# Kernel tuning notes

Measured on AMD Instinct MI355X. Metric: run time of the kernel, lower is better.

Reference implementation:

```python
import jax, jax.numpy as jnp
import numpy as np

G = 14       # patch_size
K = 4        # patch_amount
SCALE = 2    # scale_factor (undefined global in source; canonical RAM value)
C = 1
EPS = 1e-5   # torch BatchNorm1d default eps


def extract_patch(x, loc, size):
    # x: (B, C, H, W), loc in [-1, 1]. Always pad (zero-pad is value-equivalent
    # to the source's conditional padding) then gather with dynamic_slice.
    B, C_, H, W = x.shape
    pad = size // 2 + 1
    xp = jnp.pad(x, ((0, 0), (0, 0), (pad, pad), (pad, pad)))
    coords = (0.5 * ((loc + 1.0) * H)).astype(jnp.int32)  # denormalize -> (B,2) [x, y]
    x0 = coords[:, 0] - size // 2 + pad
    y0 = coords[:, 1] - size // 2 + pad

    def slice_one(img, yy, xx):
        return jax.lax.dynamic_slice(img, (0, yy, xx), (C_, size, size))

    return jax.vmap(slice_one)(xp, y0, x0)  # (B, C, size, size)


def foveate(x, loc):
    patches = []
    size = G
    for _ in range(K):
        p = extract_patch(x, loc, size)
        k = size // G
        if k > 1:  # F.avg_pool2d(p, k)
            B, C_, s, _ = p.shape
            p = p.reshape(B, C_, G, k, G, k).mean(axis=(3, 5))
        patches.append(p)
        size = int(SCALE * size)
    phi = jnp.concatenate(patches, axis=1)  # (B, K*C, G, G)
    return phi.reshape(phi.shape[0], -1)    # (B, 784)


def batchnorm(h, gamma, beta):
    # training-mode BatchNorm1d: batch stats, biased variance
    m = h.mean(axis=0)
    v = h.var(axis=0)
    return (h - m) * jax.lax.rsqrt(v + EPS) * gamma + beta


def mlp(h, W1, b1, g1, be1, W2, b2, g2, be2):
    h = jax.nn.relu(batchnorm(h @ W1 + b1, g1, be1))
    return batchnorm(h @ W2 + b2, g2, be2)


def setup_inputs() -> dict:
    key = jax.random.key(0)
    ks = jax.random.split(key, 8)
    B, H = 4096, 128
    x = jax.random.uniform(ks[0], (B, C, H, H), dtype=jnp.float32)
    loc = jax.random.uniform(ks[1], (B, 2), minval=-1.0, maxval=1.0, dtype=jnp.float32)

    def lin(k, fi, fo):
        return jax.random.normal(k, (fi, fo), dtype=jnp.float32) * 0.05

    d = {"x": x, "loc": loc}
    d["what_W1"] = lin(ks[2], 784, 128); d["what_b1"] = jnp.zeros((128,), jnp.float32)
    d["what_g1"] = jnp.ones((128,), jnp.float32); d["what_be1"] = jnp.zeros((128,), jnp.float32)
    d["what_W2"] = lin(ks[3], 128, 256); d["what_b2"] = jnp.zeros((256,), jnp.float32)
    d["what_g2"] = jnp.ones((256,), jnp.float32); d["what_be2"] = jnp.zeros((256,), jnp.float32)
    d["where_W1"] = lin(ks[4], 2, 128); d["where_b1"] = jnp.zeros((128,), jnp.float32)
    d["where_g1"] = jnp.ones((128,), jnp.float32); d["where_be1"] = jnp.zeros((128,), jnp.float32)
    d["where_W2"] = lin(ks[5], 128, 256); d["where_b2"] = jnp.zeros((256,), jnp.float32)
    d["where_g2"] = jnp.ones((256,), jnp.float32); d["where_be2"] = jnp.zeros((256,), jnp.float32)
    return d


def reference(x, loc, what_W1, what_b1, what_g1, what_be1, what_W2, what_b2, what_g2, what_be2, where_W1, where_b1, where_g1, where_be1, where_W2, where_b2, where_g2, where_be2):
    phi = foveate(x, loc)  # (B, 784)
    res_phi = mlp(phi, what_W1, what_b1, what_g1, what_be1, what_W2, what_b2, what_g2, what_be2)
    res_k = mlp(loc, where_W1, where_b1, where_g1, where_be1, where_W2, where_b2, where_g2, where_be2)
    return jax.nn.relu(res_phi + res_k)  # (B, 256)
```

## Files before the change

kernel.cpp:

```cpp
#include <hip/hip_runtime.h>
#include <hip/hip_bf16.h>

typedef __hip_bfloat16 bf16;

static constexpr int kB = 4096;
static constexpr float kEPS = 1e-5f;

__device__ __forceinline__ float cvt(float v) { return v; }
__device__ __forceinline__ float cvt(bf16 v)  { return __bfloat162float(v); }

__device__ __forceinline__ int detect_dtype(const void* __restrict__ x) {
    const bf16* p = (const bf16*)x;
    int isf32 = 0;
    for (int i = 0; i < 64; ++i) {
        float v = __bfloat162float(p[i]);
        if (!(fabsf(v) <= 2.0f)) isf32 = 1;
    }
    return isf32;
}

template <typename T>
__device__ void foveate_impl(const T* __restrict__ x, const T* __restrict__ loc,
                             float* __restrict__ phi, float* __restrict__ L1,
                             float* __restrict__ L2) {
    int b = blockIdx.x;
    float lx = cvt(loc[2 * b + 0]);
    float ly = cvt(loc[2 * b + 1]);
    int cx = (int)(0.5f * ((lx + 1.0f) * 128.0f));
    int cy = (int)(0.5f * ((ly + 1.0f) * 128.0f));
    const T* img = x + (size_t)b * 16384;
    float* ph = phi + (size_t)b * 784;

    int by0 = cy - 56, bx0 = cx - 56;
    for (int i = threadIdx.x; i < 56 * 56; i += 256) {
        int oy = i / 56, ox = i - oy * 56;
        int gy = by0 + 2 * oy, gx = bx0 + 2 * ox;
        float v00 = ((unsigned)gy       < 128u && (unsigned)gx       < 128u) ? cvt(img[gy * 128 + gx])           : 0.f;
        float v01 = ((unsigned)gy       < 128u && (unsigned)(gx + 1) < 128u) ? cvt(img[gy * 128 + gx + 1])       : 0.f;
        float v10 = ((unsigned)(gy + 1) < 128u && (unsigned)gx       < 128u) ? cvt(img[(gy + 1) * 128 + gx])     : 0.f;
        float v11 = ((unsigned)(gy + 1) < 128u && (unsigned)(gx + 1) < 128u) ? cvt(img[(gy + 1) * 128 + gx + 1]) : 0.f;
        L1[oy * 57 + ox] = ((v00 + v01) + v10) + v11;
    }
    __syncthreads();

    for (int i = threadIdx.x; i < 196; i += 256) {
        int r = i / 14, c = i % 14;
        int gy = cy - 7 + r, gx = cx - 7 + c;
        float v = ((unsigned)gy < 128u && (unsigned)gx < 128u) ? cvt(img[gy * 128 + gx]) : 0.f;
        ph[i] = v;
        ph[196 + i] = L1[(21 + r) * 57 + 21 + c] * 0.25f;
    }
    for (int i = threadIdx.x; i < 784; i += 256) {
        int oy = i / 28, ox = i % 28;
        const float* p = L1 + (2 * oy) * 57 + 2 * ox;
        L2[oy * 29 + ox] = p[0] + p[1] + p[57] + p[58];
    }
    __syncthreads();

    for (int i = threadIdx.x; i < 196; i += 256) {
        int r = i / 14, c = i % 14;
        ph[392 + i] = L2[(7 + r) * 29 + 7 + c] * 0.0625f;
        const float* p = L2 + (2 * r) * 29 + 2 * c;
        ph[588 + i] = (p[0] + p[1] + p[29] + p[30]) * 0.015625f;
    }
}

__global__ __launch_bounds__(256) void foveate_kernel(const void* __restrict__ x,
                                                      const void* __restrict__ loc,
                                                      float* __restrict__ phi,
                                                      int* __restrict__ flag) {
    __shared__ float L1[56 * 57];
    __shared__ float L2[28 * 29];
    int isf32 = detect_dtype(x);
    if (blockIdx.x == 0 && threadIdx.x == 0) *flag = isf32;
    if (isf32) foveate_impl<float>((const float*)x, (const float*)loc, phi, L1, L2);
    else       foveate_impl<bf16>((const bf16*)x, (const bf16*)loc, phi, L1, L2);
}

template <typename T>
__device__ void gemm1_impl(const float* __restrict__ A, const T* __restrict__ W,
                           const T* __restrict__ bias, float* __restrict__ C,
                           float* __restrict__ part_s, float* __restrict__ part_q,
                           float* As, float* Bs) {
    int tid = threadIdx.x;
    int tx = tid & 15, ty = tid >> 4;
    int row0 = blockIdx.y * 64, n0 = blockIdx.x * 32;

    float acc[4][2] = {};
    int am = tid >> 2;
    int ak = (tid & 3) << 2;
    int bn = tid & 31;
    int bk = tid >> 5;

    const float* Aptr = A + (size_t)(row0 + am) * 784 + ak;
    float4 av = *(const float4*)Aptr;
    float b0 = cvt(W[(size_t)bk * 128 + n0 + bn]);
    float b1 = cvt(W[(size_t)(bk + 8) * 128 + n0 + bn]);

    for (int t = 0; t < 49; ++t) {
        As[(ak + 0) * 68 + am] = av.x; As[(ak + 1) * 68 + am] = av.y;
        As[(ak + 2) * 68 + am] = av.z; As[(ak + 3) * 68 + am] = av.w;
        Bs[bk * 32 + bn] = b0; Bs[(bk + 8) * 32 + bn] = b1;
        __syncthreads();
        if (t < 48) {
            int k0 = (t + 1) << 4;
            av = *(const float4*)(Aptr + k0);
            b0 = cvt(W[(size_t)(k0 + bk) * 128 + n0 + bn]);
            b1 = cvt(W[(size_t)(k0 + bk + 8) * 128 + n0 + bn]);
        }
#pragma unroll
        for (int k = 0; k < 16; ++k) {
            float4 a  = *(const float4*)&As[k * 68 + ty * 4];
            float2 bb = *(const float2*)&Bs[k * 32 + tx * 2];
            acc[0][0] = fmaf(a.x, bb.x, acc[0][0]); acc[0][1] = fmaf(a.x, bb.y, acc[0][1]);
            acc[1][0] = fmaf(a.y, bb.x, acc[1][0]); acc[1][1] = fmaf(a.y, bb.y, acc[1][1]);
            acc[2][0] = fmaf(a.z, bb.x, acc[2][0]); acc[2][1] = fmaf(a.z, bb.y, acc[2][1]);
            acc[3][0] = fmaf(a.w, bb.x, acc[3][0]); acc[3][1] = fmaf(a.w, bb.y, acc[3][1]);
        }
        __syncthreads();
    }

    float bv0 = cvt(bias[n0 + tx * 2]);
    float bv1 = cvt(bias[n0 + tx * 2 + 1]);
    float cs0 = 0.f, cs1 = 0.f, cq0 = 0.f, cq1 = 0.f;
#pragma unroll
    for (int i = 0; i < 4; ++i) {
        float v0 = acc[i][0] + bv0, v1 = acc[i][1] + bv1;
        float2 o; o.x = v0; o.y = v1;
        *(float2*)(C + (size_t)(row0 + ty * 4 + i) * 128 + n0 + tx * 2) = o;
        cs0 += v0; cq0 += v0 * v0; cs1 += v1; cq1 += v1 * v1;
    }
    __syncthreads();
    As[ty * 32 + tx * 2]     = cs0; As[ty * 32 + tx * 2 + 1] = cs1;
    Bs[ty * 32 + tx * 2]     = cq0; Bs[ty * 32 + tx * 2 + 1] = cq1;
    __syncthreads();
    if (tid < 32) {
        float s = 0.f, q = 0.f;
#pragma unroll
        for (int p = 0; p < 16; ++p) { s += As[p * 32 + tid]; q += Bs[p * 32 + tid]; }
        part_s[(size_t)blockIdx.y * 128 + n0 + tid] = s;
        part_q[(size_t)blockIdx.y * 128 + n0 + tid] = q;
    }
}

__global__ __launch_bounds__(256) void gemm1_fused(const float* __restrict__ A,
                                                   const void* __restrict__ W,
                                                   const void* __restrict__ bias,
                                                   float* __restrict__ C,
                                                   float* __restrict__ part_s,
                                                   float* __restrict__ part_q,
                                                   const int* __restrict__ flag) {
    __shared__ __align__(16) float As[16 * 68];
    __shared__ __align__(16) float Bs[16 * 32];
    if (*flag) gemm1_impl<float>(A, (const float*)W, (const float*)bias, C, part_s, part_q, As, Bs);
    else       gemm1_impl<bf16>(A, (const bf16*)W, (const bf16*)bias, C, part_s, part_q, As, Bs);
}

template <typename T>
__device__ void where1_impl(const T* __restrict__ loc, const T* __restrict__ W,
                            const T* __restrict__ bias, float* __restrict__ q1,
                            float* __restrict__ part_s, float* __restrict__ part_q,
                            float* redS, float* redQ) {
    int c    = threadIdx.x & 127;
    int rsub = threadIdx.x >> 7;
    int rbase = blockIdx.x * 64;
    float w0 = cvt(W[c]), w1 = cvt(W[128 + c]), bv = cvt(bias[c]);
    float s = 0.f, q = 0.f;
#pragma unroll
    for (int p = 0; p < 32; ++p) {
        int r = rbase + rsub + 2 * p;
        float v = fmaf(cvt(loc[2 * r]), w0, fmaf(cvt(loc[2 * r + 1]), w1, bv));
        q1[(size_t)r * 128 + c] = v;
        s += v; q += v * v;
    }
    redS[threadIdx.x] = s; redQ[threadIdx.x] = q;
    __syncthreads();
    if (threadIdx.x < 128) {
        part_s[(size_t)blockIdx.x * 128 + c] = redS[c] + redS[c + 128];
        part_q[(size_t)blockIdx.x * 128 + c] = redQ[c] + redQ[c + 128];
    }
}

__global__ __launch_bounds__(256) void where1_fused(const void* __restrict__ loc,
                                                    const void* __restrict__ W,
                                                    const void* __restrict__ bias,
                                                    float* __restrict__ q1,
                                                    float* __restrict__ part_s,
                                                    float* __restrict__ part_q,
                                                    const int* __restrict__ flag) {
    __shared__ float redS[256], redQ[256];
    if (*flag) where1_impl<float>((const float*)loc, (const float*)W, (const float*)bias, q1, part_s, part_q, redS, redQ);
    else       where1_impl<bf16>((const bf16*)loc, (const bf16*)W, (const bf16*)bias, q1, part_s, part_q, redS, redQ);
}

template <typename T>
__device__ void fin_impl(const float* __restrict__ pS, const float* __restrict__ pQ,
                         const T* __restrict__ g, const T* __restrict__ be,
                         float* __restrict__ st) {
    int c = threadIdx.x;
    double s = 0.0, q = 0.0;
    for (int p = 0; p < 64; ++p) {
        s += (double)pS[p * 128 + c];
        q += (double)pQ[p * 128 + c];
    }
    double mean = s / 4096.0;
    double var  = q / 4096.0 - mean * mean;
    float rstd  = (float)(1.0 / sqrt(var + (double)kEPS));
    float scale = rstd * cvt(g[c]);
    st[c]       = scale;
    st[128 + c] = cvt(be[c]) - (float)mean * scale;
}

__global__ __launch_bounds__(128) void finalize_both(
        const float* __restrict__ pS1, const float* __restrict__ pQ1,
        const void* __restrict__ g1, const void* __restrict__ be1, float* __restrict__ st1,
        const float* __restrict__ pSw1, const float* __restrict__ pQw1,
        const void* __restrict__ gw1, const void* __restrict__ bew1, float* __restrict__ sw1,
        const int* __restrict__ flag) {
    const float* pS = blockIdx.x ? pSw1 : pS1;
    const float* pQ = blockIdx.x ? pQw1 : pQ1;
    const void*  g  = blockIdx.x ? gw1  : g1;
    const void*  be = blockIdx.x ? bew1 : be1;
    float* st       = blockIdx.x ? sw1  : st1;
    if (*flag) fin_impl<float>(pS, pQ, (const float*)g, (const float*)be, st);
    else       fin_impl<bf16>(pS, pQ, (const bf16*)g, (const bf16*)be, st);
}

template <typename T>
__device__ void gemm2_impl(const float* __restrict__ A, const T* __restrict__ W,
                           const T* __restrict__ bias, const float* __restrict__ st,
                           float* __restrict__ C, float* __restrict__ part_s,
                           float* __restrict__ part_q, float* As, float* Bs) {
    int tid = threadIdx.x;
    int tx = tid & 15, ty = tid >> 4;
    int row0 = blockIdx.y * 64, n0 = blockIdx.x * 64;

    float acc[4][4] = {};
    int am = tid >> 2, ak = (tid & 3) << 2;
    int bn = tid & 63, bk0 = tid >> 6;

    const float* Aptr = A + (size_t)(row0 + am) * 128 + ak;
    float4 av = *(const float4*)Aptr;
    float4 sc = *(const float4*)(st + ak);
    float4 sh = *(const float4*)(st + 128 + ak);
    float bv[4];
#pragma unroll
    for (int p = 0; p < 4; ++p) bv[p] = cvt(W[(size_t)(bk0 + 4 * p) * 256 + n0 + bn]);

    for (int t = 0; t < 8; ++t) {
        As[(ak + 0) * 68 + am] = fmaxf(fmaf(av.x, sc.x, sh.x), 0.f);
        As[(ak + 1) * 68 + am] = fmaxf(fmaf(av.y, sc.y, sh.y), 0.f);
        As[(ak + 2) * 68 + am] = fmaxf(fmaf(av.z, sc.z, sh.z), 0.f);
        As[(ak + 3) * 68 + am] = fmaxf(fmaf(av.w, sc.w, sh.w), 0.f);
#pragma unroll
        for (int p = 0; p < 4; ++p) Bs[(bk0 + 4 * p) * 64 + bn] = bv[p];
        __syncthreads();
        if (t < 7) {
            int k0 = (t + 1) << 4;
            av = *(const float4*)(Aptr + k0);
            sc = *(const float4*)(st + k0 + ak);
            sh = *(const float4*)(st + 128 + k0 + ak);
#pragma unroll
            for (int p = 0; p < 4; ++p) bv[p] = cvt(W[(size_t)(k0 + bk0 + 4 * p) * 256 + n0 + bn]);
        }
#pragma unroll
        for (int k = 0; k < 16; ++k) {
            float4 a = *(const float4*)&As[k * 68 + ty * 4];
            float4 b = *(const float4*)&Bs[k * 64 + tx * 4];
            acc[0][0] = fmaf(a.x, b.x, acc[0][0]); acc[0][1] = fmaf(a.x, b.y, acc[0][1]);
            acc[0][2] = fmaf(a.x, b.z, acc[0][2]); acc[0][3] = fmaf(a.x, b.w, acc[0][3]);
            acc[1][0] = fmaf(a.y, b.x, acc[1][0]); acc[1][1] = fmaf(a.y, b.y, acc[1][1]);
            acc[1][2] = fmaf(a.y, b.z, acc[1][2]); acc[1][3] = fmaf(a.y, b.w, acc[1][3]);
            acc[2][0] = fmaf(a.z, b.x, acc[2][0]); acc[2][1] = fmaf(a.z, b.y, acc[2][1]);
            acc[2][2] = fmaf(a.z, b.z, acc[2][2]); acc[2][3] = fmaf(a.z, b.w, acc[2][3]);
            acc[3][0] = fmaf(a.w, b.x, acc[3][0]); acc[3][1] = fmaf(a.w, b.y, acc[3][1]);
            acc[3][2] = fmaf(a.w, b.z, acc[3][2]); acc[3][3] = fmaf(a.w, b.w, acc[3][3]);
        }
        __syncthreads();
    }

    float bb[4];
#pragma unroll
    for (int j = 0; j < 4; ++j) bb[j] = cvt(bias[n0 + tx * 4 + j]);
    float cs[4] = {}, cq[4] = {};
#pragma unroll
    for (int i = 0; i < 4; ++i) {
        float v0 = acc[i][0] + bb[0], v1 = acc[i][1] + bb[1];
        float v2 = acc[i][2] + bb[2], v3 = acc[i][3] + bb[3];
        float4 o; o.x = v0; o.y = v1; o.z = v2; o.w = v3;
        cs[0] += v0; cs[1] += v1; cs[2] += v2; cs[3] += v3;
        cq[0] += v0 * v0; cq[1] += v1 * v1; cq[2] += v2 * v2; cq[3] += v3 * v3;
        *(float4*)(C + (size_t)(row0 + ty * 4 + i) * 256 + n0 + tx * 4) = o;
    }
    __syncthreads();
#pragma unroll
    for (int j = 0; j < 4; ++j) {
        As[ty * 64 + tx * 4 + j] = cs[j];
        Bs[ty * 64 + tx * 4 + j] = cq[j];
    }
    __syncthreads();
    if (tid < 64) {
        float s = 0.f, q = 0.f;
#pragma unroll
        for (int p = 0; p < 16; ++p) { s += As[p * 64 + tid]; q += Bs[p * 64 + tid]; }
        part_s[(size_t)blockIdx.y * 256 + n0 + tid] = s;
        part_q[(size_t)blockIdx.y * 256 + n0 + tid] = q;
    }
}

__global__ __launch_bounds__(256) void gemm23_fused(
        const float* __restrict__ h1, const float* __restrict__ q1,
        const void* __restrict__ wW2, const void* __restrict__ wb2,
        const void* __restrict__ hW2, const void* __restrict__ hb2,
        const float* __restrict__ st1, const float* __restrict__ sw1,
        float* __restrict__ h2, float* __restrict__ q2,
        float* __restrict__ pS2, float* __restrict__ pQ2,
        float* __restrict__ pSw2, float* __restrict__ pQw2,
        const int* __restrict__ flag) {
    __shared__ __align__(16) float As[16 * 68];
    __shared__ __align__(16) float Bs[16 * 64];
    const float* A;  const void* W; const void* bias; const float* st;
    float* C; float* ps; float* pq;
    if (blockIdx.z == 0) { A = h1; W = wW2; bias = wb2; st = st1; C = h2; ps = pS2;  pq = pQ2;  }
    else                 { A = q1; W = hW2; bias = hb2; st = sw1; C = q2; ps = pSw2; pq = pQw2; }
    if (*flag) gemm2_impl<float>(A, (const float*)W, (const float*)bias, st, C, ps, pq, As, Bs);
    else       gemm2_impl<bf16>(A, (const bf16*)W, (const bf16*)bias, st, C, ps, pq, As, Bs);
}

template <typename T>
__device__ void final_impl(const float* __restrict__ h2, const float* __restrict__ q2,
                           const float* __restrict__ pS2, const float* __restrict__ pQ2,
                           const float* __restrict__ pSw2, const float* __restrict__ pQw2,
                           const T* __restrict__ g2, const T* __restrict__ be2,
                           const T* __restrict__ gw2, const T* __restrict__ bew2,
                           T* __restrict__ out) {
    int c = threadIdx.x;
    double s = 0.0, q = 0.0, sw = 0.0, qw = 0.0;
    for (int p = 0; p < 64; ++p) {
        s  += (double)pS2[p * 256 + c];  q  += (double)pQ2[p * 256 + c];
        sw += (double)pSw2[p * 256 + c]; qw += (double)pQw2[p * 256 + c];
    }
    double mH = s / 4096.0,  vH = q / 4096.0 - mH * mH;
    double mQ = sw / 4096.0, vQ = qw / 4096.0 - mQ * mQ;
    float rH = (float)(1.0 / sqrt(vH + (double)kEPS));
    float rQ = (float)(1.0 / sqrt(vQ + (double)kEPS));
    float aH = rH * cvt(g2[c]);  float bH = cvt(be2[c])  - (float)mH * aH;
    float aQ = rQ * cvt(gw2[c]); float bQ = cvt(bew2[c]) - (float)mQ * aQ;

    for (int idx = blockIdx.x * 256 + c; idx < kB * 256; idx += 256 * 256) {
        float v = fmaxf(fmaf(h2[idx], aH, bH) + fmaf(q2[idx], aQ, bQ), 0.f);
        out[idx] = (T)v;
    }
}

__global__ __launch_bounds__(256) void final_kernel(
        const float* __restrict__ h2, const float* __restrict__ q2,
        const float* __restrict__ pS2, const float* __restrict__ pQ2,
        const float* __restrict__ pSw2, const float* __restrict__ pQw2,
        const void* __restrict__ g2, const void* __restrict__ be2,
        const void* __restrict__ gw2, const void* __restrict__ bew2,
        void* __restrict__ out, const int* __restrict__ flag) {
    if (*flag) final_impl<float>(h2, q2, pS2, pQ2, pSw2, pQw2, (const float*)g2, (const float*)be2,
                                 (const float*)gw2, (const float*)bew2, (float*)out);
    else       final_impl<bf16>(h2, q2, pS2, pQ2, pSw2, pQw2, (const bf16*)g2, (const bf16*)be2,
                                (const bf16*)gw2, (const bf16*)bew2, (bf16*)out);
}

extern "C" void kernel_launch(void* const* d_in, const int* in_sizes, int n_in,
                              void* d_out, int out_size, void* d_ws, size_t ws_size,
                              hipStream_t stream) {
    (void)in_sizes; (void)n_in; (void)out_size; (void)ws_size;
    const void* x    = d_in[0];
    const void* loc  = d_in[1];
    const void* wW1  = d_in[2];
    const void* wb1  = d_in[3];
    const void* wg1  = d_in[4];
    const void* wbe1 = d_in[5];
    const void* wW2  = d_in[6];
    const void* wb2  = d_in[7];
    const void* wg2  = d_in[8];
    const void* wbe2 = d_in[9];
    const void* hW1  = d_in[10];
    const void* hb1  = d_in[11];
    const void* hg1  = d_in[12];
    const void* hbe1 = d_in[13];
    const void* hW2  = d_in[14];
    const void* hb2  = d_in[15];
    const void* hg2  = d_in[16];
    const void* hbe2 = d_in[17];

    int*   flag = (int*)d_ws;
    float* ws   = (float*)d_ws + 16;
    float* phi  = ws;
    float* h1   = phi + (size_t)kB * 784;
    float* q1   = h1  + (size_t)kB * 128;
    float* h2   = q1  + (size_t)kB * 128;
    float* q2   = h2  + (size_t)kB * 256;
    float* st1  = q2  + (size_t)kB * 256;
    float* sw1  = st1 + 256;
    float* pS1  = sw1 + 256;
    float* pQ1  = pS1 + 8192;
    float* pSw1 = pQ1 + 8192;
    float* pQw1 = pSw1 + 8192;
    float* pS2  = phi;
    float* pQ2  = pS2 + 16384;
    float* pSw2 = pQ2 + 16384;
    float* pQw2 = pSw2 + 16384;

    foveate_kernel<<<kB, 256, 0, stream>>>(x, loc, phi, flag);

    gemm1_fused<<<dim3(4, 64), 256, 0, stream>>>(phi, wW1, wb1, h1, pS1, pQ1, flag);
    where1_fused<<<64, 256, 0, stream>>>(loc, hW1, hb1, q1, pSw1, pQw1, flag);

    finalize_both<<<2, 128, 0, stream>>>(pS1, pQ1, wg1, wbe1, st1,
                                         pSw1, pQw1, hg1, hbe1, sw1, flag);

    gemm23_fused<<<dim3(4, 64, 2), 256, 0, stream>>>(h1, q1, wW2, wb2, hW2, hb2,
                                                     st1, sw1, h2, q2,
                                                     pS2, pQ2, pSw2, pQw2, flag);

    final_kernel<<<256, 256, 0, stream>>>(h2, q2, pS2, pQ2, pSw2, pQw2,
                                          wg2, wbe2, hg2, hbe2, d_out, flag);
}
```

Baseline: 437.2 us.

## Fuse foveation with first what-GEMM and where-layer into one kernel

```diff
diff --git a/kernel.cpp b/kernel.cpp
--- a/kernel.cpp
+++ b/kernel.cpp
@@ -20,150 +20,130 @@
 }
 
 template <typename T>
-__device__ void foveate_impl(const T* __restrict__ x, const T* __restrict__ loc,
-                             float* __restrict__ phi, float* __restrict__ L1,
-                             float* __restrict__ L2) {
-    int b = blockIdx.x;
-    float lx = cvt(loc[2 * b + 0]);
-    float ly = cvt(loc[2 * b + 1]);
-    int cx = (int)(0.5f * ((lx + 1.0f) * 128.0f));
-    int cy = (int)(0.5f * ((ly + 1.0f) * 128.0f));
-    const T* img = x + (size_t)b * 16384;
-    float* ph = phi + (size_t)b * 784;
-
-    int by0 = cy - 56, bx0 = cx - 56;
-    for (int i = threadIdx.x; i < 56 * 56; i += 256) {
-        int oy = i / 56, ox = i - oy * 56;
-        int gy = by0 + 2 * oy, gx = bx0 + 2 * ox;
-        float v00 = ((unsigned)gy       < 128u && (unsigned)gx       < 128u) ? cvt(img[gy * 128 + gx])           : 0.f;
-        float v01 = ((unsigned)gy       < 128u && (unsigned)(gx + 1) < 128u) ? cvt(img[gy * 128 + gx + 1])       : 0.f;
-        float v10 = ((unsigned)(gy + 1) < 128u && (unsigned)gx       < 128u) ? cvt(img[(gy + 1) * 128 + gx])     : 0.f;
-        float v11 = ((unsigned)(gy + 1) < 128u && (unsigned)(gx + 1) < 128u) ? cvt(img[(gy + 1) * 128 + gx + 1]) : 0.f;
-        L1[oy * 57 + ox] = ((v00 + v01) + v10) + v11;
-    }
-    __syncthreads();
-
-    for (int i = threadIdx.x; i < 196; i += 256) {
-        int r = i / 14, c = i % 14;
-        int gy = cy - 7 + r, gx = cx - 7 + c;
-        float v = ((unsigned)gy < 128u && (unsigned)gx < 128u) ? cvt(img[gy * 128 + gx]) : 0.f;
-        ph[i] = v;
-        ph[196 + i] = L1[(21 + r) * 57 + 21 + c] * 0.25f;
-    }
-    for (int i = threadIdx.x; i < 784; i += 256) {
-        int oy = i / 28, ox = i % 28;
-        const float* p = L1 + (2 * oy) * 57 + 2 * ox;
-        L2[oy * 29 + ox] = p[0] + p[1] + p[57] + p[58];
-    }
-    __syncthreads();
-
-    for (int i = threadIdx.x; i < 196; i += 256) {
-        int r = i / 14, c = i % 14;
-        ph[392 + i] = L2[(7 + r) * 29 + 7 + c] * 0.0625f;
-        const float* p = L2 + (2 * r) * 29 + 2 * c;
-        ph[588 + i] = (p[0] + p[1] + p[29] + p[30]) * 0.015625f;
-    }
-}
-
-__global__ __launch_bounds__(256) void foveate_kernel(const void* __restrict__ x,
-                                                      const void* __restrict__ loc,
-                                                      float* __restrict__ phi,
-                                                      int* __restrict__ flag) {
-    __shared__ float L1[56 * 57];
-    __shared__ float L2[28 * 29];
-    int isf32 = detect_dtype(x);
-    if (blockIdx.x == 0 && threadIdx.x == 0) *flag = isf32;
-    if (isf32) foveate_impl<float>((const float*)x, (const float*)loc, phi, L1, L2);
-    else       foveate_impl<bf16>((const bf16*)x, (const bf16*)loc, phi, L1, L2);
-}
-
-template <typename T>
-__device__ void gemm1_impl(const float* __restrict__ A, const T* __restrict__ W,
-                           const T* __restrict__ bias, float* __restrict__ C,
-                           float* __restrict__ part_s, float* __restrict__ part_q,
-                           float* As, float* Bs) {
+__device__ void fovgemm_impl(const T* __restrict__ x, const T* __restrict__ loc,
+                             const T* __restrict__ W1, const T* __restrict__ b1,
+                             float* __restrict__ h1, float* __restrict__ pS,
+                             float* __restrict__ pQ, float* S) {
+    float* phiL = S;
+    float* L1b  = S + 6272;
+    float* Wt   = L1b;
     int tid = threadIdx.x;
-    int tx = tid & 15, ty = tid >> 4;
-    int row0 = blockIdx.y * 64, n0 = blockIdx.x * 32;
-
-    float acc[4][2] = {};
-    int am = tid >> 2;
-    int ak = (tid & 3) << 2;
-    int bn = tid & 31;
-    int bk = tid >> 5;
-
-    const float* Aptr = A + (size_t)(row0 + am) * 784 + ak;
-    float4 av = *(const float4*)Aptr;
-    float b0 = cvt(W[(size_t)bk * 128 + n0 + bn]);
-    float b1 = cvt(W[(size_t)(bk + 8) * 128 + n0 + bn]);
+    int bb  = blockIdx.x;
+    int r0  = bb * 8;
+
+    for (int img = 0; img < 8; ++img) {
+        int b = r0 + img;
+        float lx = cvt(loc[2 * b + 0]);
+        float ly = cvt(loc[2 * b + 1]);
+        int cx = (int)(0.5f * ((lx + 1.0f) * 128.0f));
+        int cy = (int)(0.5f * ((ly + 1.0f) * 128.0f));
+        const T* im = x + (size_t)b * 16384;
+        float* ph = phiL + img * 784;
+
+        int by0 = cy - 56, bx0 = cx - 56;
+        for (int i = tid; i < 56 * 56; i += 256) {
+            int oy = i / 56, ox = i - oy * 56;
+            int gy = by0 + 2 * oy, gx = bx0 + 2 * ox;
+            float v00 = ((unsigned)gy       < 128u && (unsigned)gx       < 128u) ? cvt(im[gy * 128 + gx])           : 0.f;
+            float v01 = ((unsigned)gy       < 128u && (unsigned)(gx + 1) < 128u) ? cvt(im[gy * 128 + gx + 1])       : 0.f;
+            float v10 = ((unsigned)(gy + 1) < 128u && (unsigned)gx       < 128u) ? cvt(im[(gy + 1) * 128 + gx])     : 0.f;
+            float v11 = ((unsigned)(gy + 1) < 128u && (unsigned)(gx + 1) < 128u) ? cvt(im[(gy + 1) * 128 + gx + 1]) : 0.f;
+            L1b[oy * 56 + ox] = ((v00 + v01) + v10) + v11;
+        }
+        __syncthreads();
+
+        for (int i = tid; i < 196; i += 256) {
+            int r = i / 14, c = i % 14;
+            int gy = cy - 7 + r, gx = cx - 7 + c;
+            ph[i] = ((unsigned)gy < 128u && (unsigned)gx < 128u) ? cvt(im[gy * 128 + gx]) : 0.f;
+            ph[196 + i] = L1b[(21 + r) * 56 + 21 + c] * 0.25f;
+
+            auto L2v = [&](int oy, int ox) {
+                const float* q = L1b + (2 * oy) * 56 + 2 * ox;
+                return ((q[0] + q[1]) + q[56]) + q[57];
+            };
+            ph[392 + i] = L2v(7 + r, 7 + c) * 0.0625f;
+            float A0 = L2v(2 * r, 2 * c),     A1 = L2v(2 * r, 2 * c + 1);
+            float A2 = L2v(2 * r + 1, 2 * c), A3 = L2v(2 * r + 1, 2 * c + 1);
+            ph[588 + i] = (((A0 + A1) + A2) + A3) * 0.015625f;
+        }
+        __syncthreads();
+    }
+
+    int tr = tid >> 5;
+    int tc = tid & 31;
+    float acc[4] = {};
+    float wreg[8];
+#pragma unroll
+    for (int j8 = 0; j8 < 8; ++j8) {
+        int j = tid + 256 * j8;
+        wreg[j8] = cvt(W1[(size_t)(j >> 7) * 128 + (j & 127)]);
+    }
 
     for (int t = 0; t < 49; ++t) {
-        As[(ak + 0) * 68 + am] = av.x; As[(ak + 1) * 68 + am] = av.y;
-        As[(ak + 2) * 68 + am] = av.z; As[(ak + 3) * 68 + am] = av.w;
-        Bs[bk * 32 + bn] = b0; Bs[(bk + 8) * 32 + bn] = b1;
+#pragma unroll
+        for (int j8 = 0; j8 < 8; ++j8) Wt[tid + 256 * j8] = wreg[j8];
         __syncthreads();
         if (t < 48) {
             int k0 = (t + 1) << 4;
-            av = *(const float4*)(Aptr + k0);
-            b0 = cvt(W[(size_t)(k0 + bk) * 128 + n0 + bn]);
-            b1 = cvt(W[(size_t)(k0 + bk + 8) * 128 + n0 + bn]);
-        }
-#pragma unroll
-        for (int k = 0; k < 16; ++k) {
-            float4 a  = *(const float4*)&As[k * 68 + ty * 4];
-            float2 bb = *(const float2*)&Bs[k * 32 + tx * 2];
-            acc[0][0] = fmaf(a.x, bb.x, acc[0][0]); acc[0][1] = fmaf(a.x, bb.y, acc[0][1]);
-            acc[1][0] = fmaf(a.y, bb.x, acc[1][0]); acc[1][1] = fmaf(a.y, bb.y, acc[1][1]);
-            acc[2][0] = fmaf(a.z, bb.x, acc[2][0]); acc[2][1] = fmaf(a.z, bb.y, acc[2][1]);
-            acc[3][0] = fmaf(a.w, bb.x, acc[3][0]); acc[3][1] = fmaf(a.w, bb.y, acc[3][1]);
-        }
-        __syncthreads();
-    }
-
-    float bv0 = cvt(bias[n0 + tx * 2]);
-    float bv1 = cvt(bias[n0 + tx * 2 + 1]);
-    float cs0 = 0.f, cs1 = 0.f, cq0 = 0.f, cq1 = 0.f;
-#pragma unroll
-    for (int i = 0; i < 4; ++i) {
-        float v0 = acc[i][0] + bv0, v1 = acc[i][1] + bv1;
-        float2 o; o.x = v0; o.y = v1;
-        *(float2*)(C + (size_t)(row0 + ty * 4 + i) * 128 + n0 + tx * 2) = o;
-        cs0 += v0; cq0 += v0 * v0; cs1 += v1; cq1 += v1 * v1;
-    }
+#pragma unroll
+            for (int j8 = 0; j8 < 8; ++j8) {
+                int j = tid + 256 * j8;
+                wreg[j8] = cvt(W1[(size_t)(k0 + (j >> 7)) * 128 + (j & 127)]);
+            }
+        }
+        const float* ap = phiL + tr * 784 + (t << 4);
+#pragma unroll
+        for (int k4 = 0; k4 < 4; ++k4) {
+            float4 a = *(const float4*)(ap + 4 * k4);
+            const float* wb = Wt + (4 * k4) * 128 + 4 * tc;
+            float4 b0 = *(const float4*)(wb);
+            float4 b1v = *(const float4*)(wb + 128);
+            float4 b2 = *(const float4*)(wb + 256);
+            float4 b3 = *(const float4*)(wb + 384);
+            acc[0] = fmaf(a.x, b0.x, acc[0]); acc[1] = fmaf(a.x, b0.y, acc[1]);
+            acc[2] = fmaf(a.x, b0.z, acc[2]); acc[3] = fmaf(a.x, b0.w, acc[3]);
+            acc[0] = fmaf(a.y, b1v.x, acc[0]); acc[1] = fmaf(a.y, b1v.y, acc[1]);
+            acc[2] = fmaf(a.y, b1v.z, acc[2]); acc[3] = fmaf(a.y, b1v.w, acc[3]);
+            acc[0] = fmaf(a.z, b2.x, acc[0]); acc[1] = fmaf(a.z, b2.y, acc[1]);
+            acc[2] = fmaf(a.z, b2.z, acc[2]); acc[3] = fmaf(a.z, b2.w, acc[3]);
+            acc[0] = fmaf(a.w, b3.x, acc[0]); acc[1] = fmaf(a.w, b3.y, acc[1]);
+            acc[2] = fmaf(a.w, b3.z, acc[2]); acc[3] = fmaf(a.w, b3.w, acc[3]);
+        }
+        __syncthreads();
+    }
+
+    float v0 = acc[0] + cvt(b1[4 * tc + 0]);
+    float v1 = acc[1] + cvt(b1[4 * tc + 1]);
+    float v2 = acc[2] + cvt(b1[4 * tc + 2]);
+    float v3 = acc[3] + cvt(b1[4 * tc + 3]);
+    float4 o; o.x = v0; o.y = v1; o.z = v2; o.w = v3;
+    *(float4*)(h1 + (size_t)(r0 + tr) * 128 + 4 * tc) = o;
+
+    float* redS = phiL;
+    float* redQ = phiL + 1024;
+    float4 cs; cs.x = v0; cs.y = v1; cs.z = v2; cs.w = v3;
+    float4 cq; cq.x = v0 * v0; cq.y = v1 * v1; cq.z = v2 * v2; cq.w = v3 * v3;
+    *(float4*)&redS[tr * 128 + 4 * tc] = cs;
+    *(float4*)&redQ[tr * 128 + 4 * tc] = cq;
     __syncthreads();
-    As[ty * 32 + tx * 2]     = cs0; As[ty * 32 + tx * 2 + 1] = cs1;
-    Bs[ty * 32 + tx * 2]     = cq0; Bs[ty * 32 + tx * 2 + 1] = cq1;
-    __syncthreads();
-    if (tid < 32) {
+    if (tid < 128) {
         float s = 0.f, q = 0.f;
 #pragma unroll
-        for (int p = 0; p < 16; ++p) { s += As[p * 32 + tid]; q += Bs[p * 32 + tid]; }
-        part_s[(size_t)blockIdx.y * 128 + n0 + tid] = s;
-        part_q[(size_t)blockIdx.y * 128 + n0 + tid] = q;
-    }
-}
-
-__global__ __launch_bounds__(256) void gemm1_fused(const float* __restrict__ A,
-                                                   const void* __restrict__ W,
-                                                   const void* __restrict__ bias,
-                                                   float* __restrict__ C,
-                                                   float* __restrict__ part_s,
-                                                   float* __restrict__ part_q,
-                                                   const int* __restrict__ flag) {
-    __shared__ __align__(16) float As[16 * 68];
-    __shared__ __align__(16) float Bs[16 * 32];
-    if (*flag) gemm1_impl<float>(A, (const float*)W, (const float*)bias, C, part_s, part_q, As, Bs);
-    else       gemm1_impl<bf16>(A, (const bf16*)W, (const bf16*)bias, C, part_s, part_q, As, Bs);
+        for (int p = 0; p < 8; ++p) { s += redS[p * 128 + tid]; q += redQ[p * 128 + tid]; }
+        pS[(size_t)bb * 128 + tid] = s;
+        pQ[(size_t)bb * 128 + tid] = q;
+    }
 }
 
 template <typename T>
 __device__ void where1_impl(const T* __restrict__ loc, const T* __restrict__ W,
                             const T* __restrict__ bias, float* __restrict__ q1,
                             float* __restrict__ part_s, float* __restrict__ part_q,
-                            float* redS, float* redQ) {
+                            float* redS, float* redQ, int wb) {
     int c    = threadIdx.x & 127;
     int rsub = threadIdx.x >> 7;
-    int rbase = blockIdx.x * 64;
+    int rbase = wb * 64;
     float w0 = cvt(W[c]), w1 = cvt(W[128 + c]), bv = cvt(bias[c]);
     float s = 0.f, q = 0.f;
 #pragma unroll
@@ -176,30 +156,45 @@
     redS[threadIdx.x] = s; redQ[threadIdx.x] = q;
     __syncthreads();
     if (threadIdx.x < 128) {
-        part_s[(size_t)blockIdx.x * 128 + c] = redS[c] + redS[c + 128];
-        part_q[(size_t)blockIdx.x * 128 + c] = redQ[c] + redQ[c + 128];
-    }
-}
-
-__global__ __launch_bounds__(256) void where1_fused(const void* __restrict__ loc,
-                                                    const void* __restrict__ W,
-                                                    const void* __restrict__ bias,
-                                                    float* __restrict__ q1,
-                                                    float* __restrict__ part_s,
-                                                    float* __restrict__ part_q,
-                                                    const int* __restrict__ flag) {
-    __shared__ float redS[256], redQ[256];
-    if (*flag) where1_impl<float>((const float*)loc, (const float*)W, (const float*)bias, q1, part_s, part_q, redS, redQ);
-    else       where1_impl<bf16>((const bf16*)loc, (const bf16*)W, (const bf16*)bias, q1, part_s, part_q, redS, redQ);
+        part_s[(size_t)wb * 128 + c] = redS[c] + redS[c + 128];
+        part_q[(size_t)wb * 128 + c] = redQ[c] + redQ[c + 128];
+    }
+}
+
+__global__ __launch_bounds__(256) void fused1(
+        const void* __restrict__ x, const void* __restrict__ loc,
+        const void* __restrict__ wW1, const void* __restrict__ wb1,
+        const void* __restrict__ hW1, const void* __restrict__ hb1,
+        float* __restrict__ h1, float* __restrict__ q1,
+        float* __restrict__ pS1, float* __restrict__ pQ1,
+        float* __restrict__ pSw1, float* __restrict__ pQw1,
+        int* __restrict__ flag) {
+    __shared__ __align__(16) float S[8 * 784 + 56 * 56];
+    int isf32 = detect_dtype(x);
+    if (blockIdx.x == 0 && threadIdx.x == 0) *flag = isf32;
+    if (blockIdx.x < 512) {
+        if (isf32) fovgemm_impl<float>((const float*)x, (const float*)loc,
+                                       (const float*)wW1, (const float*)wb1,
+                                       h1, pS1, pQ1, S);
+        else       fovgemm_impl<bf16>((const bf16*)x, (const bf16*)loc,
+                                      (const bf16*)wW1, (const bf16*)wb1,
+                                      h1, pS1, pQ1, S);
+    } else {
+        int wb = blockIdx.x - 512;
+        if (isf32) where1_impl<float>((const float*)loc, (const float*)hW1,
+                                      (const float*)hb1, q1, pSw1, pQw1, S, S + 256, wb);
+        else       where1_impl<bf16>((const bf16*)loc, (const bf16*)hW1,
+                                     (const bf16*)hb1, q1, pSw1, pQw1, S, S + 256, wb);
+    }
 }
 
 template <typename T>
 __device__ void fin_impl(const float* __restrict__ pS, const float* __restrict__ pQ,
                          const T* __restrict__ g, const T* __restrict__ be,
-                         float* __restrict__ st) {
+                         float* __restrict__ st, int nparts) {
     int c = threadIdx.x;
     double s = 0.0, q = 0.0;
-    for (int p = 0; p < 64; ++p) {
+    for (int p = 0; p < nparts; ++p) {
         s += (double)pS[p * 128 + c];
         q += (double)pQ[p * 128 + c];
     }
@@ -222,8 +217,9 @@
     const void*  g  = blockIdx.x ? gw1  : g1;
     const void*  be = blockIdx.x ? bew1 : be1;
     float* st       = blockIdx.x ? sw1  : st1;
-    if (*flag) fin_impl<float>(pS, pQ, (const float*)g, (const float*)be, st);
-    else       fin_impl<bf16>(pS, pQ, (const bf16*)g, (const bf16*)be, st);
+    int nparts      = blockIdx.x ? 64   : 512;
+    if (*flag) fin_impl<float>(pS, pQ, (const float*)g, (const float*)be, st, nparts);
+    else       fin_impl<bf16>(pS, pQ, (const bf16*)g, (const bf16*)be, st, nparts);
 }
 
 template <typename T>
@@ -391,26 +387,23 @@
 
     int*   flag = (int*)d_ws;
     float* ws   = (float*)d_ws + 16;
-    float* phi  = ws;
-    float* h1   = phi + (size_t)kB * 784;
+    float* h1   = ws;
     float* q1   = h1  + (size_t)kB * 128;
     float* h2   = q1  + (size_t)kB * 128;
     float* q2   = h2  + (size_t)kB * 256;
     float* st1  = q2  + (size_t)kB * 256;
     float* sw1  = st1 + 256;
     float* pS1  = sw1 + 256;
-    float* pQ1  = pS1 + 8192;
-    float* pSw1 = pQ1 + 8192;
+    float* pQ1  = pS1 + 65536;
+    float* pSw1 = pQ1 + 65536;
     float* pQw1 = pSw1 + 8192;
-    float* pS2  = phi;
+    float* pS2  = pQw1 + 8192;
     float* pQ2  = pS2 + 16384;
     float* pSw2 = pQ2 + 16384;
     float* pQw2 = pSw2 + 16384;
 
-    foveate_kernel<<<kB, 256, 0, stream>>>(x, loc, phi, flag);
-
-    gemm1_fused<<<dim3(4, 64), 256, 0, stream>>>(phi, wW1, wb1, h1, pS1, pQ1, flag);
-    where1_fused<<<64, 256, 0, stream>>>(loc, hW1, hb1, q1, pSw1, pQw1, flag);
+    fused1<<<576, 256, 0, stream>>>(x, loc, wW1, wb1, hW1, hb1,
+                                    h1, q1, pS1, pQ1, pSw1, pQw1, flag);
 
     finalize_both<<<2, 128, 0, stream>>>(pS1, pQ1, wg1, wbe1, st1,
                                          pSw1, pQw1, hg1, hbe1, sw1, flag);
```

Measured after the change: 576.9 us. 1.32x slower.

## Merge where1 into foveate launch and shrink gemm1 tiles to double grid

Applied to the files above, without the earlier changes.

```diff
diff --git a/kernel.cpp b/kernel.cpp
--- a/kernel.cpp
+++ b/kernel.cpp
@@ -65,74 +65,105 @@
     }
 }
 
-__global__ __launch_bounds__(256) void foveate_kernel(const void* __restrict__ x,
-                                                      const void* __restrict__ loc,
-                                                      float* __restrict__ phi,
-                                                      int* __restrict__ flag) {
+template <typename T>
+__device__ void where1_impl(const T* __restrict__ loc, const T* __restrict__ W,
+                            const T* __restrict__ bias, float* __restrict__ q1,
+                            float* __restrict__ part_s, float* __restrict__ part_q,
+                            float* redS, float* redQ, int wb) {
+    int c    = threadIdx.x & 127;
+    int rsub = threadIdx.x >> 7;
+    int rbase = wb * 64;
+    float w0 = cvt(W[c]), w1 = cvt(W[128 + c]), bv = cvt(bias[c]);
+    float s = 0.f, q = 0.f;
+#pragma unroll
+    for (int p = 0; p < 32; ++p) {
+        int r = rbase + rsub + 2 * p;
+        float v = fmaf(cvt(loc[2 * r]), w0, fmaf(cvt(loc[2 * r + 1]), w1, bv));
+        q1[(size_t)r * 128 + c] = v;
+        s += v; q += v * v;
+    }
+    redS[threadIdx.x] = s; redQ[threadIdx.x] = q;
+    __syncthreads();
+    if (threadIdx.x < 128) {
+        part_s[(size_t)wb * 128 + c] = redS[c] + redS[c + 128];
+        part_q[(size_t)wb * 128 + c] = redQ[c] + redQ[c + 128];
+    }
+}
+
+__global__ __launch_bounds__(256) void foveate_kernel(
+        const void* __restrict__ x, const void* __restrict__ loc,
+        const void* __restrict__ hW1, const void* __restrict__ hb1,
+        float* __restrict__ phi, float* __restrict__ q1,
+        float* __restrict__ pSw1, float* __restrict__ pQw1,
+        int* __restrict__ flag) {
     __shared__ float L1[56 * 57];
     __shared__ float L2[28 * 29];
     int isf32 = detect_dtype(x);
     if (blockIdx.x == 0 && threadIdx.x == 0) *flag = isf32;
-    if (isf32) foveate_impl<float>((const float*)x, (const float*)loc, phi, L1, L2);
-    else       foveate_impl<bf16>((const bf16*)x, (const bf16*)loc, phi, L1, L2);
+    if (blockIdx.x < 4096) {
+        if (isf32) foveate_impl<float>((const float*)x, (const float*)loc, phi, L1, L2);
+        else       foveate_impl<bf16>((const bf16*)x, (const bf16*)loc, phi, L1, L2);
+    } else {
+        int wb = blockIdx.x - 4096;
+        if (isf32) where1_impl<float>((const float*)loc, (const float*)hW1,
+                                      (const float*)hb1, q1, pSw1, pQw1, L1, L2, wb);
+        else       where1_impl<bf16>((const bf16*)loc, (const bf16*)hW1,
+                                     (const bf16*)hb1, q1, pSw1, pQw1, L1, L2, wb);
+    }
 }
 
 template <typename T>
 __device__ void gemm1_impl(const float* __restrict__ A, const T* __restrict__ W,
                            const T* __restrict__ bias, float* __restrict__ C,
                            float* __restrict__ part_s, float* __restrict__ part_q,
-                           float* As, float* Bs) {
+                           float* As , float* Bs ) {
     int tid = threadIdx.x;
     int tx = tid & 15, ty = tid >> 4;
-    int row0 = blockIdx.y * 64, n0 = blockIdx.x * 32;
-
-    float acc[4][2] = {};
-    int am = tid >> 2;
-    int ak = (tid & 3) << 2;
-    int bn = tid & 31;
-    int bk = tid >> 5;
+    int row0 = blockIdx.y * 32, n0 = blockIdx.x * 32;
+
+    float a00 = 0.f, a01 = 0.f, a10 = 0.f, a11 = 0.f;
+    int am = tid & 31;
+    int ak = (tid >> 5) * 2;
+    int bc = (tid & 15) * 2;
+    int bk = tid >> 4;
 
     const float* Aptr = A + (size_t)(row0 + am) * 784 + ak;
-    float4 av = *(const float4*)Aptr;
-    float b0 = cvt(W[(size_t)bk * 128 + n0 + bn]);
-    float b1 = cvt(W[(size_t)(bk + 8) * 128 + n0 + bn]);
+    float2 av = *(const float2*)Aptr;
+    float w0 = cvt(W[(size_t)bk * 128 + n0 + bc]);
+    float w1 = cvt(W[(size_t)bk * 128 + n0 + bc + 1]);
 
     for (int t = 0; t < 49; ++t) {
-        As[(ak + 0) * 68 + am] = av.x; As[(ak + 1) * 68 + am] = av.y;
-        As[(ak + 2) * 68 + am] = av.z; As[(ak + 3) * 68 + am] = av.w;
-        Bs[bk * 32 + bn] = b0; Bs[(bk + 8) * 32 + bn] = b1;
+        As[(ak + 0) * 34 + am] = av.x;
+        As[(ak + 1) * 34 + am] = av.y;
+        *(float2*)&Bs[bk * 32 + bc] = make_float2(w0, w1);
         __syncthreads();
         if (t < 48) {
             int k0 = (t + 1) << 4;
-            av = *(const float4*)(Aptr + k0);
-            b0 = cvt(W[(size_t)(k0 + bk) * 128 + n0 + bn]);
-            b1 = cvt(W[(size_t)(k0 + bk + 8) * 128 + n0 + bn]);
+            av = *(const float2*)(Aptr + k0);
+            w0 = cvt(W[(size_t)(k0 + bk) * 128 + n0 + bc]);
+            w1 = cvt(W[(size_t)(k0 + bk) * 128 + n0 + bc + 1]);
         }
 #pragma unroll
         for (int k = 0; k < 16; ++k) {
-            float4 a  = *(const float4*)&As[k * 68 + ty * 4];
-            float2 bb = *(const float2*)&Bs[k * 32 + tx * 2];
-            acc[0][0] = fmaf(a.x, bb.x, acc[0][0]); acc[0][1] = fmaf(a.x, bb.y, acc[0][1]);
-            acc[1][0] = fmaf(a.y, bb.x, acc[1][0]); acc[1][1] = fmaf(a.y, bb.y, acc[1][1]);
-            acc[2][0] = fmaf(a.z, bb.x, acc[2][0]); acc[2][1] = fmaf(a.z, bb.y, acc[2][1]);
-            acc[3][0] = fmaf(a.w, bb.x, acc[3][0]); acc[3][1] = fmaf(a.w, bb.y, acc[3][1]);
+            float2 a = *(const float2*)&As[k * 34 + ty * 2];
+            float2 b = *(const float2*)&Bs[k * 32 + tx * 2];
+            a00 = fmaf(a.x, b.x, a00); a01 = fmaf(a.x, b.y, a01);
+            a10 = fmaf(a.y, b.x, a10); a11 = fmaf(a.y, b.y, a11);
         }
         __syncthreads();
     }
 
     float bv0 = cvt(bias[n0 + tx * 2]);
     float bv1 = cvt(bias[n0 + tx * 2 + 1]);
-    float cs0 = 0.f, cs1 = 0.f, cq0 = 0.f, cq1 = 0.f;
-#pragma unroll
-    for (int i = 0; i < 4; ++i) {
-        float v0 = acc[i][0] + bv0, v1 = acc[i][1] + bv1;
-        float2 o; o.x = v0; o.y = v1;
-        *(float2*)(C + (size_t)(row0 + ty * 4 + i) * 128 + n0 + tx * 2) = o;
-        cs0 += v0; cq0 += v0 * v0; cs1 += v1; cq1 += v1 * v1;
-    }
-    __syncthreads();
-    As[ty * 32 + tx * 2]     = cs0; As[ty * 32 + tx * 2 + 1] = cs1;
-    Bs[ty * 32 + tx * 2]     = cq0; Bs[ty * 32 + tx * 2 + 1] = cq1;
+    float v00 = a00 + bv0, v01 = a01 + bv1;
+    float v10 = a10 + bv0, v11 = a11 + bv1;
+    *(float2*)(C + (size_t)(row0 + ty * 2 + 0) * 128 + n0 + tx * 2) = make_float2(v00, v01);
+    *(float2*)(C + (size_t)(row0 + ty * 2 + 1) * 128 + n0 + tx * 2) = make_float2(v10, v11);
+
+    __syncthreads();
+    *(float2*)&As[ty * 32 + tx * 2] = make_float2(v00 + v10, v01 + v11);
+    *(float2*)&Bs[ty * 32 + tx * 2] = make_float2(v00 * v00 + v10 * v10,
+                                                  v01 * v01 + v11 * v11);
     __syncthreads();
     if (tid < 32) {
         float s = 0.f, q = 0.f;
@@ -150,56 +181,19 @@
                                                    float* __restrict__ part_s,
                                                    float* __restrict__ part_q,
                                                    const int* __restrict__ flag) {
-    __shared__ __align__(16) float As[16 * 68];
+    __shared__ __align__(16) float As[16 * 34];
     __shared__ __align__(16) float Bs[16 * 32];
     if (*flag) gemm1_impl<float>(A, (const float*)W, (const float*)bias, C, part_s, part_q, As, Bs);
     else       gemm1_impl<bf16>(A, (const bf16*)W, (const bf16*)bias, C, part_s, part_q, As, Bs);
 }
 
 template <typename T>
-__device__ void where1_impl(const T* __restrict__ loc, const T* __restrict__ W,
-                            const T* __restrict__ bias, float* __restrict__ q1,
-                            float* __restrict__ part_s, float* __restrict__ part_q,
-                            float* redS, float* redQ) {
-    int c    = threadIdx.x & 127;
-    int rsub = threadIdx.x >> 7;
-    int rbase = blockIdx.x * 64;
-    float w0 = cvt(W[c]), w1 = cvt(W[128 + c]), bv = cvt(bias[c]);
-    float s = 0.f, q = 0.f;
-#pragma unroll
-    for (int p = 0; p < 32; ++p) {
-        int r = rbase + rsub + 2 * p;
-        float v = fmaf(cvt(loc[2 * r]), w0, fmaf(cvt(loc[2 * r + 1]), w1, bv));
-        q1[(size_t)r * 128 + c] = v;
-        s += v; q += v * v;
-    }
-    redS[threadIdx.x] = s; redQ[threadIdx.x] = q;
-    __syncthreads();
-    if (threadIdx.x < 128) {
-        part_s[(size_t)blockIdx.x * 128 + c] = redS[c] + redS[c + 128];
-        part_q[(size_t)blockIdx.x * 128 + c] = redQ[c] + redQ[c + 128];
-    }
-}
-
-__global__ __launch_bounds__(256) void where1_fused(const void* __restrict__ loc,
-                                                    const void* __restrict__ W,
-                                                    const void* __restrict__ bias,
-                                                    float* __restrict__ q1,
-                                                    float* __restrict__ part_s,
-                                                    float* __restrict__ part_q,
-                                                    const int* __restrict__ flag) {
-    __shared__ float redS[256], redQ[256];
-    if (*flag) where1_impl<float>((const float*)loc, (const float*)W, (const float*)bias, q1, part_s, part_q, redS, redQ);
-    else       where1_impl<bf16>((const bf16*)loc, (const bf16*)W, (const bf16*)bias, q1, part_s, part_q, redS, redQ);
-}
-
-template <typename T>
 __device__ void fin_impl(const float* __restrict__ pS, const float* __restrict__ pQ,
                          const T* __restrict__ g, const T* __restrict__ be,
-                         float* __restrict__ st) {
+                         float* __restrict__ st, int nparts) {
     int c = threadIdx.x;
     double s = 0.0, q = 0.0;
-    for (int p = 0; p < 64; ++p) {
+    for (int p = 0; p < nparts; ++p) {
         s += (double)pS[p * 128 + c];
         q += (double)pQ[p * 128 + c];
     }
@@ -222,8 +216,9 @@
     const void*  g  = blockIdx.x ? gw1  : g1;
     const void*  be = blockIdx.x ? bew1 : be1;
     float* st       = blockIdx.x ? sw1  : st1;
-    if (*flag) fin_impl<float>(pS, pQ, (const float*)g, (const float*)be, st);
-    else       fin_impl<bf16>(pS, pQ, (const bf16*)g, (const bf16*)be, st);
+    int nparts      = blockIdx.x ? 64   : 128;
+    if (*flag) fin_impl<float>(pS, pQ, (const float*)g, (const float*)be, st, nparts);
+    else       fin_impl<bf16>(pS, pQ, (const bf16*)g, (const bf16*)be, st, nparts);
 }
 
 template <typename T>
@@ -399,18 +394,18 @@
     float* st1  = q2  + (size_t)kB * 256;
     float* sw1  = st1 + 256;
     float* pS1  = sw1 + 256;
-    float* pQ1  = pS1 + 8192;
-    float* pSw1 = pQ1 + 8192;
+    float* pQ1  = pS1 + 16384;
+    float* pSw1 = pQ1 + 16384;
     float* pQw1 = pSw1 + 8192;
     float* pS2  = phi;
     float* pQ2  = pS2 + 16384;
     float* pSw2 = pQ2 + 16384;
     float* pQw2 = pSw2 + 16384;
 
-    foveate_kernel<<<kB, 256, 0, stream>>>(x, loc, phi, flag);
-
-    gemm1_fused<<<dim3(4, 64), 256, 0, stream>>>(phi, wW1, wb1, h1, pS1, pQ1, flag);
-    where1_fused<<<64, 256, 0, stream>>>(loc, hW1, hb1, q1, pSw1, pQw1, flag);
+    foveate_kernel<<<4160, 256, 0, stream>>>(x, loc, hW1, hb1,
+                                             phi, q1, pSw1, pQw1, flag);
+
+    gemm1_fused<<<dim3(4, 128), 256, 0, stream>>>(phi, wW1, wb1, h1, pS1, pQ1, flag);
 
     finalize_both<<<2, 128, 0, stream>>>(pS1, pQ1, wg1, wbe1, st1,
                                          pSw1, pQw1, hg1, hbe1, sw1, flag);
```

After: 463.2 us. 1.06x slower.
